# Kernel tuning notes

Hardware: AMD Instinct MI355X
Metric: run time of the kernel (lower is better)

The kernel has to match this reference:

```python
import jax, jax.numpy as jnp
import numpy as np

B, S, D = 4, 2048, 1024
E, K, H = 8, 2, 1408
LB_WEIGHT = 0.01


def setup_inputs() -> dict:
    key = jax.random.key(0)
    ks = jax.random.split(key, 7)
    sc = 0.02
    return {
        "x": jax.random.normal(ks[0], (B, S, D), dtype=jnp.float32),
        "Wr": jax.random.normal(ks[1], (D, E), dtype=jnp.float32) * sc,
        "Wg": jax.random.normal(ks[2], (E, D, H), dtype=jnp.float32) * sc,
        "Wu": jax.random.normal(ks[3], (E, D, H), dtype=jnp.float32) * sc,
        "Wx": jax.random.normal(ks[4], (E, D, H), dtype=jnp.float32) * sc,
        "Wd": jax.random.normal(ks[5], (E, H, D), dtype=jnp.float32) * sc,
        "alpha": jnp.ones((E,), dtype=jnp.float32),
    }


def _moe(x, Wr, Wg, Wu, Wx, Wd, alpha):
    Bv, Sv, Dv = x.shape
    xf = x.reshape(-1, Dv)  # [T, D]
    router_probs = jax.nn.softmax(xf @ Wr, axis=-1)  # [T, E]
    topk_p, topk_i = jax.lax.top_k(router_probs, K)  # [T, K]
    topk_p = topk_p / jnp.sum(topk_p, axis=-1, keepdims=True)
    # dense combine weights [T, E]; zero for non-selected experts
    combine = jnp.sum(topk_p[..., None] * jax.nn.one_hot(topk_i, E, dtype=xf.dtype), axis=1)
    out = jnp.zeros_like(xf)
    for e in range(E):
        gate = xf @ Wg[e]
        up = xf @ Wu[e]
        expand = xf @ Wx[e]
        ga = jax.nn.silu(gate) * up
        ea = jax.nn.silu(expand) * up
        combined = alpha[e] * ga + (1.0 - alpha[e]) * ea
        eo = combined @ Wd[e]  # [T, D]
        out = out + eo * combine[:, e:e + 1]
    # load balancing loss: mse(mean usage, 1/E)
    usage = jnp.mean(router_probs, axis=0)
    lb = LB_WEIGHT * jnp.mean((usage - 1.0 / E) ** 2)
    return out.reshape(Bv, Sv, Dv), lb


def reference(x, Wr, Wg, Wu, Wx, Wd, alpha):
    return _moe(x, Wr, Wg, Wu, Wx, Wd, alpha)
```

## Files before the change

kernel.cpp:

```cpp
#include <hip/hip_runtime.h>
#include <stdint.h>

typedef unsigned short u16;
typedef __attribute__((ext_vector_type(8))) short short8;
typedef __attribute__((ext_vector_type(4))) float floatx4;

#define T_TOK 8192
#define DM 1024
#define NE 8
#define HD 1408
#define LDA 72

__device__ __forceinline__ float bf2f(u16 u) {
  union { float f; uint32_t i; } v; v.i = ((uint32_t)u) << 16; return v.f;
}
__device__ __forceinline__ u16 f2bf(float f) {
  union { float f; uint32_t i; } v; v.f = f;
  uint32_t r = v.i + 0x7fffu + ((v.i >> 16) & 1u);
  return (u16)(r >> 16);
}
__device__ __forceinline__ void llds16(const void* g, void* l) {
  __builtin_amdgcn_global_load_lds((const __attribute__((address_space(1))) void*)g,
                                   (__attribute__((address_space(3))) void*)l, 16, 0, 0);
}
__device__ __forceinline__ floatx4 mfma16(short8 a, short8 b, floatx4 c) {
  return __builtin_amdgcn_mfma_f32_16x16x32_bf16(a, b, c, 0, 0, 0);
}

__global__ void detect_k(const u16* __restrict__ xraw, int* __restrict__ flag) {
  int lane = threadIdx.x & 63;
  u16 w = xraw[lane * 2];
  int ex = (w >> 7) & 0xFF;
  bool hit = (ex >= 100 && ex <= 135);
  unsigned long long m = __ballot(hit);
  if (lane == 0) *flag = (__popcll(m) >= 40) ? 1 : 0;
}

__global__ void conv_alpha_k(const void* __restrict__ araw, u16* __restrict__ ab,
                             const int* __restrict__ flag) {
  int f = *flag;
  if (threadIdx.x < NE) {
    ab[threadIdx.x] = f ? ((const u16*)araw)[threadIdx.x]
                        : f2bf(((const float*)araw)[threadIdx.x]);
  }
}

__global__ __launch_bounds__(256) void conv_x_k(const void* __restrict__ xraw,
                                                u16* __restrict__ xb,
                                                const int* __restrict__ flag) {
  if (*flag) return;
  size_t base = ((size_t)blockIdx.x * 256 + threadIdx.x) * 8;
  const float* s = (const float*)xraw + base;
  float4 v0 = *(const float4*)s;
  float4 v1 = *(const float4*)(s + 4);
  ushort4 o0, o1;
  o0.x = f2bf(v0.x); o0.y = f2bf(v0.y); o0.z = f2bf(v0.z); o0.w = f2bf(v0.w);
  o1.x = f2bf(v1.x); o1.y = f2bf(v1.y); o1.z = f2bf(v1.z); o1.w = f2bf(v1.w);
  *(ushort4*)(xb + base) = o0;
  *(ushort4*)(xb + base + 4) = o1;
}

__global__ __launch_bounds__(256) void transpose_k(
    const void* __restrict__ src, u16* __restrict__ dst, int R, int C,
    const u16* __restrict__ alphab, int mode, const int* __restrict__ flag) {
  int e = blockIdx.z;
  if (mode) {
    float a = bf2f(alphab[e]);
    if (mode == 1 && a == 1.0f) return;
    if (mode == 2 && a == 0.0f) return;
  }
  int f = *flag;
  __shared__ u16 tile[64][65];
  u16* d = dst + (size_t)e * R * C;
  int c0 = blockIdx.x * 64, r0 = blockIdx.y * 64;
  int tx = threadIdx.x & 63, ty = threadIdx.x >> 6;
  if (f) {
    const u16* s = (const u16*)src + (size_t)e * R * C;
    for (int i = ty; i < 64; i += 4)
      tile[i][tx] = s[(size_t)(r0 + i) * C + (c0 + tx)];
  } else {
    const float* s = (const float*)src + (size_t)e * R * C;
    for (int i = ty; i < 64; i += 4)
      tile[i][tx] = f2bf(s[(size_t)(r0 + i) * C + (c0 + tx)]);
  }
  __syncthreads();
  int i2 = threadIdx.x >> 5, tx2 = threadIdx.x & 31;
  for (int ii = i2; ii < 64; ii += 8) {
    ushort2 v; v.x = tile[2 * tx2][ii]; v.y = tile[2 * tx2 + 1][ii];
    *(ushort2*)&d[(size_t)(c0 + ii) * R + r0 + 2 * tx2] = v;
  }
}

__global__ __launch_bounds__(256) void rdot_k(
    const void* __restrict__ x, const void* __restrict__ Wr,
    float* __restrict__ probs, const int* __restrict__ flag) {
  int wave = threadIdx.x >> 6, lane = threadIdx.x & 63;
  int t = blockIdx.x * 4 + wave;
  int f = *flag;
  float acc[8];
  #pragma unroll
  for (int e = 0; e < 8; e++) acc[e] = 0.0f;
  if (f) {
    const u16* xr = (const u16*)x + (size_t)t * DM;
    const u16* wr = (const u16*)Wr;
    #pragma unroll
    for (int i = 0; i < 16; i++) {
      int d = i * 64 + lane;
      float xv = bf2f(xr[d]);
      uint4 wv = *(const uint4*)(wr + (size_t)d * 8);
      acc[0] += xv * bf2f((u16)(wv.x & 0xffff));
      acc[1] += xv * bf2f((u16)(wv.x >> 16));
      acc[2] += xv * bf2f((u16)(wv.y & 0xffff));
      acc[3] += xv * bf2f((u16)(wv.y >> 16));
      acc[4] += xv * bf2f((u16)(wv.z & 0xffff));
      acc[5] += xv * bf2f((u16)(wv.z >> 16));
      acc[6] += xv * bf2f((u16)(wv.w & 0xffff));
      acc[7] += xv * bf2f((u16)(wv.w >> 16));
    }
  } else {
    const float* xr = (const float*)x + (size_t)t * DM;
    const float* wr = (const float*)Wr;
    #pragma unroll
    for (int i = 0; i < 16; i++) {
      int d = i * 64 + lane;
      float xv = xr[d];
      float4 w0 = *(const float4*)(wr + (size_t)d * 8);
      float4 w1 = *(const float4*)(wr + (size_t)d * 8 + 4);
      acc[0] += xv * w0.x; acc[1] += xv * w0.y;
      acc[2] += xv * w0.z; acc[3] += xv * w0.w;
      acc[4] += xv * w1.x; acc[5] += xv * w1.y;
      acc[6] += xv * w1.z; acc[7] += xv * w1.w;
    }
  }
  #pragma unroll
  for (int e = 0; e < 8; e++) {
    #pragma unroll
    for (int s = 32; s; s >>= 1) acc[e] += __shfl_xor(acc[e], s, 64);
  }
  float mx = acc[0];
  #pragma unroll
  for (int e = 1; e < 8; e++) mx = fmaxf(mx, acc[e]);
  float p[8], sum = 0.0f;
  #pragma unroll
  for (int e = 0; e < 8; e++) { p[e] = __expf(acc[e] - mx); sum += p[e]; }
  float inv = 1.0f / sum;
  if (lane < 8) probs[(size_t)t * 8 + lane] = p[lane] * inv;
}

__global__ __launch_bounds__(256) void build_k(
    const float* __restrict__ probs, int* __restrict__ counts,
    float* __restrict__ usage, int* __restrict__ tok_ids,
    float* __restrict__ tok_w) {
  __shared__ int sCnt[8];
  __shared__ int sBase[8];
  __shared__ float sUse[8];
  int tid = threadIdx.x;
  if (tid < 8) { sCnt[tid] = 0; sUse[tid] = 0.0f; }
  __syncthreads();

  int t = blockIdx.x * 256 + tid;
  float4 p0 = *(const float4*)(probs + (size_t)t * 8);
  float4 p1 = *(const float4*)(probs + (size_t)t * 8 + 4);
  float p[8] = {p0.x, p0.y, p0.z, p0.w, p1.x, p1.y, p1.z, p1.w};

  #pragma unroll
  for (int e = 0; e < 8; e++) {
    float v = p[e];
    #pragma unroll
    for (int s = 32; s; s >>= 1) v += __shfl_xor(v, s, 64);
    if ((tid & 63) == 0) atomicAdd(&sUse[e], v);
  }

  int e0 = 0;
  #pragma unroll
  for (int e = 1; e < 8; e++) if (p[e] > p[e0]) e0 = e;
  int e1 = (e0 == 0) ? 1 : 0;
  #pragma unroll
  for (int e = 0; e < 8; e++) if (e != e0 && p[e] > p[e1]) e1 = e;
  float s2 = 1.0f / (p[e0] + p[e1]);

  int s0 = atomicAdd(&sCnt[e0], 1);
  int s1 = atomicAdd(&sCnt[e1], 1);
  __syncthreads();
  if (tid < 8) {
    sBase[tid] = atomicAdd(&counts[tid], sCnt[tid]);
    atomicAdd(&usage[tid], sUse[tid]);
  }
  __syncthreads();
  int i0 = sBase[e0] + s0;
  tok_ids[e0 * T_TOK + i0] = t; tok_w[e0 * T_TOK + i0] = p[e0] * s2;
  int i1 = sBase[e1] + s1;
  tok_ids[e1 * T_TOK + i1] = t; tok_w[e1 * T_TOK + i1] = p[e1] * s2;
}

__global__ void scan_k(const int* __restrict__ counts, int* __restrict__ offs) {
  if (threadIdx.x == 0) {
    int s = 0;
    for (int e = 0; e < 8; e++) { offs[e] = s; s += counts[e]; }
    offs[8] = s;
  }
}

__global__ __launch_bounds__(256, 2) void stageA2_k(
    const void* __restrict__ xraw, const u16* __restrict__ xb,
    const u16* __restrict__ WgT, const u16* __restrict__ WuT,
    const u16* __restrict__ alphab, const int* __restrict__ counts,
    const int* __restrict__ offs, const int* __restrict__ tok_ids,
    u16* __restrict__ comb, const int* __restrict__ flag) {
  int e = blockIdx.z;
  float aE = bf2f(alphab[e]);
  if (aE != 1.0f) return;
  int cnt = counts[e];
  int m0 = blockIdx.y * 128;
  if (m0 >= cnt) return;
  int h0 = blockIdx.x * 128;
  int rem = cnt - m0;
  const u16* x = (*flag) ? (const u16*)xraw : xb;

  alignas(16) __shared__ u16 sA[128 * 64];
  alignas(16) __shared__ u16 sG[128 * 64];
  alignas(16) __shared__ u16 sU[128 * 64];
  __shared__ int sTok[128];

  int tid = threadIdx.x;
  if (tid < 128)
    sTok[tid] = tok_ids[e * T_TOK + ((tid < rem) ? (m0 + tid) : m0)];
  __syncthreads();

  const u16* wg = WgT + (size_t)e * HD * DM;
  const u16* wu = WuT + (size_t)e * HD * DM;

  int lane = tid & 63, wave = tid >> 6;
  int wm = wave & 1, wn = wave >> 1;
  int lr = lane & 15, quad = lane >> 4;

  const u16* aptr[4]; const u16* gptr[4]; const u16* uptr[4];
  u16 *dA[4], *dG[4], *dU[4];
  #pragma unroll
  for (int i = 0; i < 4; i++) {
    int f = tid + 256 * i;
    int row = f >> 3, seg = f & 7;
    aptr[i] = x + (size_t)sTok[row] * DM + seg * 8;
    gptr[i] = wg + (size_t)(h0 + row) * DM + seg * 8;
    uptr[i] = wu + (size_t)(h0 + row) * DM + seg * 8;
    dA[i] = &sA[f * 8]; dG[i] = &sG[f * 8]; dU[i] = &sU[f * 8];
  }

  floatx4 accG[4][4], accU[4][4];
  #pragma unroll
  for (int i = 0; i < 4; i++)
    #pragma unroll
    for (int j = 0; j < 4; j++) { accG[i][j] = (floatx4)0.0f; accU[i][j] = (floatx4)0.0f; }

  for (int kt = 0; kt < DM / 64; kt++) {
    int k0 = kt * 64;
    __syncthreads();
    #pragma unroll
    for (int i = 0; i < 4; i++) llds16(aptr[i] + k0, dA[i]);
    #pragma unroll
    for (int i = 0; i < 4; i++) llds16(uptr[i] + k0, dU[i]);
    #pragma unroll
    for (int i = 0; i < 4; i++) llds16(gptr[i] + k0, dG[i]);
    __syncthreads();
    #pragma unroll
    for (int kk = 0; kk < 2; kk++) {
      int kb = kk * 32 + quad * 8;
      short8 a[4];
      #pragma unroll
      for (int i = 0; i < 4; i++)
        a[i] = *(const short8*)&sA[(wm * 64 + i * 16 + lr) * 64 + kb];
      #pragma unroll
      for (int j = 0; j < 4; j++) {
        int nb = (wn * 64 + j * 16 + lr) * 64 + kb;
        short8 bu = *(const short8*)&sU[nb];
        #pragma unroll
        for (int i = 0; i < 4; i++) accU[i][j] = mfma16(a[i], bu, accU[i][j]);
        short8 bg = *(const short8*)&sG[nb];
        #pragma unroll
        for (int i = 0; i < 4; i++) accG[i][j] = mfma16(a[i], bg, accG[i][j]);
      }
    }
  }

  size_t rbase = (size_t)(offs[e] + m0);
  #pragma unroll
  for (int i = 0; i < 4; i++) {
    #pragma unroll
    for (int r = 0; r < 4; r++) {
      int row = wm * 64 + i * 16 + quad * 4 + r;
      if (row < rem) {
        u16* cp = comb + (rbase + row) * HD + h0 + wn * 64 + lr;
        #pragma unroll
        for (int j = 0; j < 4; j++) {
          float g = accG[i][j][r], u = accU[i][j][r];
          float sg = g / (1.0f + __expf(-g));
          cp[j * 16] = f2bf(u * sg);
        }
      }
    }
  }
}

__global__ __launch_bounds__(256, 2) void stageA_k(
    const void* __restrict__ xraw, const u16* __restrict__ xb,
    const u16* __restrict__ WgT, const u16* __restrict__ WuT,
    const u16* __restrict__ WxT, const u16* __restrict__ alphab,
    const int* __restrict__ counts, const int* __restrict__ offs,
    const int* __restrict__ tok_ids, u16* __restrict__ comb,
    const int* __restrict__ flag) {
  int e = blockIdx.z;
  float aE = bf2f(alphab[e]);
  if (aE == 1.0f) return;
  int cnt = counts[e];
  int m0 = blockIdx.y * 128;
  if (m0 >= cnt) return;
  int h0 = blockIdx.x * 64;
  int rem = cnt - m0;
  const u16* x = (*flag) ? (const u16*)xraw : xb;

  alignas(16) __shared__ u16 sA[128 * LDA];
  alignas(16) __shared__ u16 sG[64 * LDA];
  alignas(16) __shared__ u16 sU[64 * LDA];
  alignas(16) __shared__ u16 sX[64 * LDA];
  __shared__ int sTok[128];

  int tid = threadIdx.x;
  if (tid < 128)
    sTok[tid] = tok_ids[e * T_TOK + ((tid < rem) ? (m0 + tid) : m0)];
  __syncthreads();

  bool needG = (aE != 0.0f);

  const u16* wg = WgT + (size_t)e * HD * DM;
  const u16* wu = WuT + (size_t)e * HD * DM;
  const u16* wx = WxT + (size_t)e * HD * DM;

  int lane = tid & 63, wave = tid >> 6;
  int wm = wave & 1, wn = wave >> 1;
  int lr = lane & 15, quad = lane >> 4;

  int rowA[4], segA[4], rowW[2], segW[2];
  #pragma unroll
  for (int i = 0; i < 4; i++) { int f = tid + 256 * i; rowA[i] = f >> 3; segA[i] = f & 7; }
  #pragma unroll
  for (int i = 0; i < 2; i++) { int f = tid + 256 * i; rowW[i] = f >> 3; segW[i] = f & 7; }

  floatx4 accG[4][2], accU[4][2], accX[4][2];
  #pragma unroll
  for (int i = 0; i < 4; i++)
    #pragma unroll
    for (int j = 0; j < 2; j++) {
      accG[i][j] = (floatx4)0.0f; accU[i][j] = (floatx4)0.0f; accX[i][j] = (floatx4)0.0f;
    }

  short8 rA[4], rU[2], rG[2], rX[2];
  #pragma unroll
  for (int i = 0; i < 4; i++)
    rA[i] = *(const short8*)(x + (size_t)sTok[rowA[i]] * DM + segA[i] * 8);
  #pragma unroll
  for (int i = 0; i < 2; i++) {
    size_t go = (size_t)(h0 + rowW[i]) * DM + segW[i] * 8;
    rU[i] = *(const short8*)(wu + go);
    if (needG) rG[i] = *(const short8*)(wg + go);
    rX[i] = *(const short8*)(wx + go);
  }

  const int NK = DM / 64;
  for (int kt = 0; kt < NK; kt++) {
    __syncthreads();
    #pragma unroll
    for (int i = 0; i < 4; i++)
      *(short8*)&sA[rowA[i] * LDA + segA[i] * 8] = rA[i];
    #pragma unroll
    for (int i = 0; i < 2; i++) {
      *(short8*)&sU[rowW[i] * LDA + segW[i] * 8] = rU[i];
      if (needG) *(short8*)&sG[rowW[i] * LDA + segW[i] * 8] = rG[i];
      *(short8*)&sX[rowW[i] * LDA + segW[i] * 8] = rX[i];
    }
    __syncthreads();
    if (kt + 1 < NK) {
      int k0 = (kt + 1) * 64;
      #pragma unroll
      for (int i = 0; i < 4; i++)
        rA[i] = *(const short8*)(x + (size_t)sTok[rowA[i]] * DM + k0 + segA[i] * 8);
      #pragma unroll
      for (int i = 0; i < 2; i++) {
        size_t go = (size_t)(h0 + rowW[i]) * DM + k0 + segW[i] * 8;
        rU[i] = *(const short8*)(wu + go);
        if (needG) rG[i] = *(const short8*)(wg + go);
        rX[i] = *(const short8*)(wx + go);
      }
    }
    #pragma unroll
    for (int kk = 0; kk < 2; kk++) {
      int kb = kk * 32 + quad * 8;
      short8 a[4];
      #pragma unroll
      for (int i = 0; i < 4; i++)
        a[i] = *(const short8*)&sA[(wm * 64 + i * 16 + lr) * LDA + kb];
      #pragma unroll
      for (int j = 0; j < 2; j++) {
        int nb = (wn * 32 + j * 16 + lr) * LDA + kb;
        short8 bu = *(const short8*)&sU[nb];
        #pragma unroll
        for (int i = 0; i < 4; i++) accU[i][j] = mfma16(a[i], bu, accU[i][j]);
        if (needG) {
          short8 bg = *(const short8*)&sG[nb];
          #pragma unroll
          for (int i = 0; i < 4; i++) accG[i][j] = mfma16(a[i], bg, accG[i][j]);
        }
        short8 bx = *(const short8*)&sX[nb];
        #pragma unroll
        for (int i = 0; i < 4; i++) accX[i][j] = mfma16(a[i], bx, accX[i][j]);
      }
    }
  }

  float a1 = aE, a2 = 1.0f - aE;
  size_t rbase = (size_t)(offs[e] + m0);
  #pragma unroll
  for (int i = 0; i < 4; i++) {
    #pragma unroll
    for (int r = 0; r < 4; r++) {
      int row = wm * 64 + i * 16 + quad * 4 + r;
      if (row < rem) {
        u16* cp = comb + (rbase + row) * HD + h0 + wn * 32 + lr;
        #pragma unroll
        for (int j = 0; j < 2; j++) {
          float g = accG[i][j][r], u = accU[i][j][r], xx = accX[i][j][r];
          float sg = g / (1.0f + __expf(-g));
          float sx = xx / (1.0f + __expf(-xx));
          cp[j * 16] = f2bf(u * (a1 * sg + a2 * sx));
        }
      }
    }
  }
}

__global__ __launch_bounds__(256, 2) void stageB_k(
    const u16* __restrict__ comb, const u16* __restrict__ WdT,
    const int* __restrict__ counts, const int* __restrict__ offs,
    const int* __restrict__ tok_ids, const float* __restrict__ tok_w,
    float* __restrict__ accb) {
  int e = blockIdx.z;
  int cnt = counts[e];
  int m0 = blockIdx.y * 128;
  if (m0 >= cnt) return;
  int d0 = blockIdx.x * 128;
  int rem = cnt - m0;

  alignas(16) __shared__ u16 sA[128 * 64];
  alignas(16) __shared__ u16 sB[128 * 64];
  __shared__ int sTok[128];
  __shared__ float sW[128];

  int tid = threadIdx.x;
  if (tid < 128) {
    bool v = tid < rem;
    sTok[tid] = v ? tok_ids[e * T_TOK + m0 + tid] : 0;
    sW[tid] = v ? tok_w[e * T_TOK + m0 + tid] : 0.0f;
  }
  __syncthreads();

  const u16* ca = comb + (size_t)(offs[e] + m0) * HD;
  const u16* wd = WdT + (size_t)e * DM * HD;

  int lane = tid & 63, wave = tid >> 6;
  int wm = wave & 1, wn = wave >> 1;
  int lr = lane & 15, quad = lane >> 4;

  const u16* aptr[4]; const u16* bptr[4];
  u16 *dA[4], *dB[4];
  #pragma unroll
  for (int i = 0; i < 4; i++) {
    int f = tid + 256 * i;
    int row = f >> 3, seg = f & 7;
    int rc = (row < rem) ? row : 0;
    aptr[i] = ca + (size_t)rc * HD + seg * 8;
    bptr[i] = wd + (size_t)(d0 + row) * HD + seg * 8;
    dA[i] = &sA[f * 8]; dB[i] = &sB[f * 8];
  }

  floatx4 acc[4][4];
  #pragma unroll
  for (int i = 0; i < 4; i++)
    #pragma unroll
    for (int j = 0; j < 4; j++) acc[i][j] = (floatx4)0.0f;

  for (int kt = 0; kt < HD / 64; kt++) {
    int k0 = kt * 64;
    __syncthreads();
    #pragma unroll
    for (int i = 0; i < 4; i++) llds16(aptr[i] + k0, dA[i]);
    #pragma unroll
    for (int i = 0; i < 4; i++) llds16(bptr[i] + k0, dB[i]);
    __syncthreads();
    #pragma unroll
    for (int kk = 0; kk < 2; kk++) {
      int kb = kk * 32 + quad * 8;
      short8 a[4];
      #pragma unroll
      for (int i = 0; i < 4; i++)
        a[i] = *(const short8*)&sA[(wm * 64 + i * 16 + lr) * 64 + kb];
      #pragma unroll
      for (int j = 0; j < 4; j++) {
        short8 b = *(const short8*)&sB[(wn * 64 + j * 16 + lr) * 64 + kb];
        #pragma unroll
        for (int i = 0; i < 4; i++) acc[i][j] = mfma16(a[i], b, acc[i][j]);
      }
    }
  }

  #pragma unroll
  for (int i = 0; i < 4; i++) {
    #pragma unroll
    for (int r = 0; r < 4; r++) {
      int row = wm * 64 + i * 16 + quad * 4 + r;
      if (row < rem) {
        int t = sTok[row];
        float w = sW[row];
        float* orow = accb + (size_t)t * DM + d0 + wn * 64 + lr;
        #pragma unroll
        for (int j = 0; j < 4; j++)
          atomicAdd(&orow[j * 16], acc[i][j][r] * w);
      }
    }
  }
}

__global__ __launch_bounds__(256) void finalize_k(
    const float* __restrict__ accb, const float* __restrict__ usage,
    void* __restrict__ out, const int* __restrict__ flag) {
  int f = *flag;
  size_t idx = (size_t)blockIdx.x * 256 + threadIdx.x;
  float4 v = ((const float4*)accb)[idx];
  float lb = 0.0f;
  if (idx == 0) {
    for (int e = 0; e < 8; e++) {
      float d = usage[e] * (1.0f / 8192.0f) - 0.125f;
      lb += d * d;
    }
    lb *= 0.01f * 0.125f;
  }
  if (f) {
    u16* o = (u16*)out;
    ushort4 ov;
    ov.x = f2bf(v.x); ov.y = f2bf(v.y); ov.z = f2bf(v.z); ov.w = f2bf(v.w);
    ((ushort4*)o)[idx] = ov;
    if (idx == 0) o[(size_t)T_TOK * DM] = f2bf(lb);
  } else {
    float* o = (float*)out;
    ((float4*)o)[idx] = v;
    if (idx == 0) o[(size_t)T_TOK * DM] = lb;
  }
}

extern "C" void kernel_launch(void* const* d_in, const int* in_sizes, int n_in,
                              void* d_out, int out_size, void* d_ws, size_t ws_size,
                              hipStream_t stream) {
  const void* x  = d_in[0];
  const void* Wr = d_in[1];
  const void* Wg = d_in[2];
  const void* Wu = d_in[3];
  const void* Wx = d_in[4];
  const void* Wd = d_in[5];
  const void* al = d_in[6];
  char* ws = (char*)d_ws;

  int*   counts  = (int*)(ws + 0);
  float* usage   = (float*)(ws + 32);
  int*   flag    = (int*)(ws + 64);
  float* accb    = (float*)(ws + 128);
  int*   offs    = (int*)(ws + 33554560);
  int*   tok_ids = (int*)(ws + 33554624);
  float* tok_w   = (float*)(ws + 33816768);
  u16*   alphab  = (u16*)(ws + 34078912);
  u16*   xb      = (u16*)(ws + 34078976);
  u16*   comb    = (u16*)(ws + 50856192);
  u16*   WgT     = (u16*)(ws + 96993536);
  u16*   WuT     = (u16*)(ws + 120062208);
  u16*   WdT     = (u16*)(ws + 143130880);
  float* probs   = (float*)(ws + 166199552);
  u16*   WxT     = (u16*)(ws + 166461696);

  hipMemsetAsync(ws, 0, 33554560, stream);

  dim3 b256(256, 1, 1);
  detect_k<<<dim3(1), dim3(64), 0, stream>>>((const u16*)x, flag);
  conv_alpha_k<<<dim3(1), dim3(64), 0, stream>>>(al, alphab, flag);
  conv_x_k<<<dim3(4096), b256, 0, stream>>>(x, xb, flag);
  transpose_k<<<dim3(HD / 64, DM / 64, NE), b256, 0, stream>>>(Wg, WgT, DM, HD, alphab, 2, flag);
  transpose_k<<<dim3(HD / 64, DM / 64, NE), b256, 0, stream>>>(Wu, WuT, DM, HD, alphab, 0, flag);
  transpose_k<<<dim3(HD / 64, DM / 64, NE), b256, 0, stream>>>(Wx, WxT, DM, HD, alphab, 1, flag);
  transpose_k<<<dim3(DM / 64, HD / 64, NE), b256, 0, stream>>>(Wd, WdT, HD, DM, alphab, 0, flag);
  rdot_k<<<dim3(T_TOK / 4), b256, 0, stream>>>(x, Wr, probs, flag);
  build_k<<<dim3(T_TOK / 256), b256, 0, stream>>>(probs, counts, usage, tok_ids, tok_w);
  scan_k<<<dim3(1), dim3(64), 0, stream>>>(counts, offs);
  stageA2_k<<<dim3(HD / 128, T_TOK / 128, NE), b256, 0, stream>>>(
      x, xb, WgT, WuT, alphab, counts, offs, tok_ids, comb, flag);
  stageA_k<<<dim3(HD / 64, T_TOK / 128, NE), b256, 0, stream>>>(
      x, xb, WgT, WuT, WxT, alphab, counts, offs, tok_ids, comb, flag);
  stageB_k<<<dim3(DM / 128, T_TOK / 128, NE), b256, 0, stream>>>(
      comb, WdT, counts, offs, tok_ids, tok_w, accb);
  finalize_k<<<dim3((T_TOK * DM / 4) / 256), b256, 0, stream>>>(accb, usage, d_out, flag);
}
```

Before: 508.6 us.

## Vectorize weight transpose, XOR-swizzle LDS tiles, and interleave expert block order

The weight transpose kernel now loads and stores in 4- and 8-element vectors instead of scalars, cutting memory transaction count. The stageA2 and stageB GEMMs XOR-swizzle the 16-byte segment position within each LDS row, which is meant to avoid bank conflicts on the short8 fragment reads. They also use a flat 1D grid with the expert index in the low bits, so the 8 experts are interleaved across CUs and early-exit blocks are spread out instead of clumped. The swizzle has to stay consistent between the global-to-LDS writes and the fragment reads. The transposed column reads in the transpose kernel may still hit LDS bank conflicts.

```diff
diff --git a/kernel.cpp b/kernel.cpp
--- a/kernel.cpp
+++ b/kernel.cpp
@@ -70,24 +70,32 @@
     if (mode == 2 && a == 0.0f) return;
   }
   int f = *flag;
-  __shared__ u16 tile[64][65];
+  __shared__ u16 tile[64][68];
   u16* d = dst + (size_t)e * R * C;
   int c0 = blockIdx.x * 64, r0 = blockIdx.y * 64;
-  int tx = threadIdx.x & 63, ty = threadIdx.x >> 6;
+  int tid = threadIdx.x;
+  int r = tid >> 4, c4 = (tid & 15) * 4;
   if (f) {
     const u16* s = (const u16*)src + (size_t)e * R * C;
-    for (int i = ty; i < 64; i += 4)
-      tile[i][tx] = s[(size_t)(r0 + i) * C + (c0 + tx)];
+    for (int rr = r; rr < 64; rr += 16) {
+      ushort4 v = *(const ushort4*)&s[(size_t)(r0 + rr) * C + c0 + c4];
+      *(ushort4*)&tile[rr][c4] = v;
+    }
   } else {
     const float* s = (const float*)src + (size_t)e * R * C;
-    for (int i = ty; i < 64; i += 4)
-      tile[i][tx] = f2bf(s[(size_t)(r0 + i) * C + (c0 + tx)]);
+    for (int rr = r; rr < 64; rr += 16) {
+      float4 v = *(const float4*)&s[(size_t)(r0 + rr) * C + c0 + c4];
+      ushort4 o; o.x = f2bf(v.x); o.y = f2bf(v.y); o.z = f2bf(v.z); o.w = f2bf(v.w);
+      *(ushort4*)&tile[rr][c4] = o;
+    }
   }
   __syncthreads();
-  int i2 = threadIdx.x >> 5, tx2 = threadIdx.x & 31;
-  for (int ii = i2; ii < 64; ii += 8) {
-    ushort2 v; v.x = tile[2 * tx2][ii]; v.y = tile[2 * tx2 + 1][ii];
-    *(ushort2*)&d[(size_t)(c0 + ii) * R + r0 + 2 * tx2] = v;
+  int rg = (tid & 7) * 8, ii = tid >> 3;
+  for (int i2 = ii; i2 < 64; i2 += 32) {
+    short8 v;
+    #pragma unroll
+    for (int t = 0; t < 8; t++) ((u16*)&v)[t] = tile[rg + t][i2];
+    *(short8*)&d[(size_t)(c0 + i2) * R + r0 + rg] = v;
   }
 }
 
@@ -207,13 +215,15 @@
     const u16* __restrict__ alphab, const int* __restrict__ counts,
     const int* __restrict__ offs, const int* __restrict__ tok_ids,
     u16* __restrict__ comb, const int* __restrict__ flag) {
-  int e = blockIdx.z;
+  int bid = blockIdx.x;
+  int e = bid & 7;
   float aE = bf2f(alphab[e]);
   if (aE != 1.0f) return;
+  int t2 = bid >> 3;
+  int h0 = (t2 % (HD / 128)) * 128;
+  int m0 = (t2 / (HD / 128)) * 128;
   int cnt = counts[e];
-  int m0 = blockIdx.y * 128;
   if (m0 >= cnt) return;
-  int h0 = blockIdx.x * 128;
   int rem = cnt - m0;
   const u16* x = (*flag) ? (const u16*)xraw : xb;
 
@@ -239,7 +249,8 @@
   #pragma unroll
   for (int i = 0; i < 4; i++) {
     int f = tid + 256 * i;
-    int row = f >> 3, seg = f & 7;
+    int row = f >> 3;
+    int seg = (f & 7) ^ (row & 7);
     aptr[i] = x + (size_t)sTok[row] * DM + seg * 8;
     gptr[i] = wg + (size_t)(h0 + row) * DM + seg * 8;
     uptr[i] = wu + (size_t)(h0 + row) * DM + seg * 8;
@@ -264,14 +275,14 @@
     __syncthreads();
     #pragma unroll
     for (int kk = 0; kk < 2; kk++) {
-      int kb = kk * 32 + quad * 8;
+      int slot = ((kk * 4 + quad) ^ (lr & 7)) * 8;
       short8 a[4];
       #pragma unroll
       for (int i = 0; i < 4; i++)
-        a[i] = *(const short8*)&sA[(wm * 64 + i * 16 + lr) * 64 + kb];
+        a[i] = *(const short8*)&sA[(wm * 64 + i * 16 + lr) * 64 + slot];
       #pragma unroll
       for (int j = 0; j < 4; j++) {
-        int nb = (wn * 64 + j * 16 + lr) * 64 + kb;
+        int nb = (wn * 64 + j * 16 + lr) * 64 + slot;
         short8 bu = *(const short8*)&sU[nb];
         #pragma unroll
         for (int i = 0; i < 4; i++) accU[i][j] = mfma16(a[i], bu, accU[i][j]);
@@ -442,11 +453,13 @@
     const int* __restrict__ counts, const int* __restrict__ offs,
     const int* __restrict__ tok_ids, const float* __restrict__ tok_w,
     float* __restrict__ accb) {
-  int e = blockIdx.z;
+  int bid = blockIdx.x;
+  int e = bid & 7;
+  int t2 = bid >> 3;
+  int d0 = (t2 % (DM / 128)) * 128;
+  int m0 = (t2 / (DM / 128)) * 128;
   int cnt = counts[e];
-  int m0 = blockIdx.y * 128;
   if (m0 >= cnt) return;
-  int d0 = blockIdx.x * 128;
   int rem = cnt - m0;
 
   alignas(16) __shared__ u16 sA[128 * 64];
@@ -474,7 +487,8 @@
   #pragma unroll
   for (int i = 0; i < 4; i++) {
     int f = tid + 256 * i;
-    int row = f >> 3, seg = f & 7;
+    int row = f >> 3;
+    int seg = (f & 7) ^ (row & 7);
     int rc = (row < rem) ? row : 0;
     aptr[i] = ca + (size_t)rc * HD + seg * 8;
     bptr[i] = wd + (size_t)(d0 + row) * HD + seg * 8;
@@ -497,14 +511,14 @@
     __syncthreads();
     #pragma unroll
     for (int kk = 0; kk < 2; kk++) {
-      int kb = kk * 32 + quad * 8;
+      int slot = ((kk * 4 + quad) ^ (lr & 7)) * 8;
       short8 a[4];
       #pragma unroll
       for (int i = 0; i < 4; i++)
-        a[i] = *(const short8*)&sA[(wm * 64 + i * 16 + lr) * 64 + kb];
+        a[i] = *(const short8*)&sA[(wm * 64 + i * 16 + lr) * 64 + slot];
       #pragma unroll
       for (int j = 0; j < 4; j++) {
-        short8 b = *(const short8*)&sB[(wn * 64 + j * 16 + lr) * 64 + kb];
+        short8 b = *(const short8*)&sB[(wn * 64 + j * 16 + lr) * 64 + slot];
         #pragma unroll
         for (int i = 0; i < 4; i++) acc[i][j] = mfma16(a[i], b, acc[i][j]);
       }
@@ -596,11 +610,11 @@
   rdot_k<<<dim3(T_TOK / 4), b256, 0, stream>>>(x, Wr, probs, flag);
   build_k<<<dim3(T_TOK / 256), b256, 0, stream>>>(probs, counts, usage, tok_ids, tok_w);
   scan_k<<<dim3(1), dim3(64), 0, stream>>>(counts, offs);
-  stageA2_k<<<dim3(HD / 128, T_TOK / 128, NE), b256, 0, stream>>>(
+  stageA2_k<<<dim3(NE * (HD / 128) * (T_TOK / 128)), b256, 0, stream>>>(
       x, xb, WgT, WuT, alphab, counts, offs, tok_ids, comb, flag);
   stageA_k<<<dim3(HD / 64, T_TOK / 128, NE), b256, 0, stream>>>(
       x, xb, WgT, WuT, WxT, alphab, counts, offs, tok_ids, comb, flag);
-  stageB_k<<<dim3(DM / 128, T_TOK / 128, NE), b256, 0, stream>>>(
+  stageB_k<<<dim3(NE * (DM / 128) * (T_TOK / 128)), b256, 0, stream>>>(
       comb, WdT, counts, offs, tok_ids, tok_w, accb);
   finalize_k<<<dim3((T_TOK * DM / 4) / 256), b256, 0, stream>>>(accb, usage, d_out, flag);
 }
```

Result: faster. 469.4 us (-7.7%).
